# Kernel optimization log

Hardware: AMD Instinct MI355X
Metric: run time of the kernel (lower is better)

## Reference

```python
import math
import jax, jax.numpy as jnp
import numpy as np

H = 8  # num_heads


def setup_inputs() -> dict:
    key = jax.random.key(0)
    ks = jax.random.split(key, 9)
    B, N = 2, 4096
    Cc, C, Cs = 512, 512, 128  # in_channels, hidden_size, in_channels//4
    f = lambda k, shp: jax.random.normal(k, shp, dtype=jnp.float32) * 0.02
    return {
        "s": f(ks[0], (B, N, Cc)),
        "h": f(ks[1], (B, N, Cs)),
        "sh": f(ks[2], (B, N, C)),
        "temperature": jnp.full((H, 1, 1), 0.1, jnp.float32),
        "temperature2": jnp.full((H, 1, 1), 0.1, jnp.float32),
        "Wq_c": f(ks[3], (Cc, Cc)),
        "Wq_s": f(ks[4], (C, C)),
        "Wk_c": f(ks[5], (C, C)),
        "Wv_c": f(ks[6], (C, C)),
        "Wk_s": f(ks[7], (C, C)),
        "Wv_s": f(ks[8], (Cs, Cs)),
    }


def reference(s, h, sh, temperature, temperature2, Wq_c, Wq_s, Wk_c, Wv_c, Wk_s, Wv_s):
    B, N, C = sh.shape
    Cc = s.shape[2]
    Cs = h.shape[2]
    dc, d, ds = Cc // H, C // H, Cs // H

    # torch nn.Linear(bias=False): y = x @ W.T ; reshapes replicate torch's
    # direct reshape(B, H, N, d) layout (no (B,N,H,d)+transpose head split).
    q_c = (s @ Wq_c.T).reshape(B, H, N, dc).swapaxes(-1, -2)  # (B,H,dc,N)
    q_s = (sh @ Wq_s.T).reshape(B, H, N, d)
    k_c = (sh @ Wk_c.T).reshape(B, H, N, d)
    v_c = (sh @ Wv_c.T).reshape(B, H, N, d)
    k_s = (sh @ Wk_s.T).reshape(B, H, N, d)
    v_s = (h @ Wv_s.T).reshape(B, H, N, ds)

    # Channel branch: (B,H,dc,N) @ (B,H,N,d) -> (B,H,dc,d)
    attn_ca = (q_c @ k_c) / math.sqrt(d) * temperature
    attn_ca = jax.nn.softmax(attn_ca, axis=-1)
    x_ca = (attn_ca @ v_c.swapaxes(-2, -1)).reshape(B, N, Cc)  # (B,H,dc,N)->(B,N,Cc)

    # Spatial branch: (B,H,N,d) @ (B,H,d,N) -> (B,H,N,N)
    attn_sa = (q_s @ k_s.swapaxes(-2, -1)) / math.sqrt(d) * temperature2
    attn_sa = jax.nn.softmax(attn_sa, axis=-1)
    x_sa = (attn_sa @ v_s).reshape(B, N, Cs)  # (B,H,N,ds)->(B,N,Cs)

    return jnp.concatenate([x_ca, x_sa], axis=2)  # (B,N,Cc+Cs)
```

## Files before the change

kernel.cpp:

```cpp
#include <hip/hip_runtime.h>


typedef __attribute__((ext_vector_type(8))) __bf16 bf16x8;
typedef __attribute__((ext_vector_type(4))) __bf16 bf16x4;
typedef __attribute__((ext_vector_type(4))) float  f32x4;
typedef __attribute__((ext_vector_type(4))) short  s16x4;

#define LOG2E 1.44269504088896340736f

static __device__ __forceinline__ int is_bf16_io(const unsigned* p)
{
    const unsigned w = p[0];
    return (w >> 16) == (w & 0xffffu);
}

static __device__ __forceinline__ f32x4 mfma16(bf16x4 a, bf16x4 b, f32x4 c)
{
#if __has_builtin(__builtin_amdgcn_mfma_f32_16x16x16bf16_1k)
    union { bf16x4 h; s16x4 s; } ua, ub;
    ua.h = a; ub.h = b;
    return __builtin_amdgcn_mfma_f32_16x16x16bf16_1k(ua.s, ub.s, c, 0, 0, 0);
#elif __has_builtin(__builtin_amdgcn_mfma_f32_16x16x16_bf16)
    return __builtin_amdgcn_mfma_f32_16x16x16_bf16(a, b, c, 0, 0, 0);
#else
    asm("v_mfma_f32_16x16x16_bf16 %0, %1, %2, %0" : "+v"(c) : "v"(a), "v"(b));
    return c;
#endif
}

struct ProjArgs {
    const void* X[6];
    const void* W[6];
    __bf16*     Y[6];
    int         K[6];
    int         yofs[7];
    int         ng;
};

__global__ __launch_bounds__(256) void proj_gemm(ProjArgs args,
                                                 const unsigned* __restrict__ tw)
{
    __shared__ __align__(16) union ShMem {
        struct { __bf16 A[2][128][72]; __bf16 B[2][128][72]; } s;
        __bf16 C[4][64][72];
    } sm;

    const int bf = is_bf16_io(tw);
    const int by = blockIdx.y;
    int g = 0;
    while (by >= args.yofs[g + 1]) ++g;
    const int n0 = (by - args.yofs[g]) * 128;
    const int N  = (args.yofs[g + 1] - args.yofs[g]) * 128;
    const int K  = args.K[g];
    const void* X = args.X[g];
    const void* W = args.W[g];
    __bf16*     Y = args.Y[g];

    const int m0 = blockIdx.x * 128;
    const int t = threadIdx.x;
    const int wave = t >> 6, lane = t & 63;
    const int wr = (wave >> 1) * 64, wc = (wave & 1) * 64;
    const int m16 = lane & 15, quad = lane >> 4;

    f32x4 acc[4][4];
#pragma unroll
    for (int i = 0; i < 4; ++i)
#pragma unroll
        for (int j = 0; j < 4; ++j) acc[i][j] = (f32x4){0.f, 0.f, 0.f, 0.f};

    if (bf) {
        const __bf16* Xb = (const __bf16*)X;
        const __bf16* Wb = (const __bf16*)W;
        bf16x8 pa[4], pb[4];
        auto load = [&](int k0) {
#pragma unroll
            for (int i = 0; i < 4; ++i) {
                const int idx = t + i * 256, row = idx >> 3, off = (idx & 7) * 8;
                pa[i] = *(const bf16x8*)(Xb + (size_t)(m0 + row) * K + k0 + off);
            }
#pragma unroll
            for (int i = 0; i < 4; ++i) {
                const int idx = t + i * 256, row = idx >> 3, off = (idx & 7) * 8;
                pb[i] = *(const bf16x8*)(Wb + (size_t)(n0 + row) * K + k0 + off);
            }
        };
        auto store = [&](int bi) {
#pragma unroll
            for (int i = 0; i < 4; ++i) {
                const int idx = t + i * 256, row = idx >> 3, off = (idx & 7) * 8;
                *(bf16x8*)&sm.s.A[bi][row][off] = pa[i];
            }
#pragma unroll
            for (int i = 0; i < 4; ++i) {
                const int idx = t + i * 256, row = idx >> 3, off = (idx & 7) * 8;
                *(bf16x8*)&sm.s.B[bi][row][off] = pb[i];
            }
        };
        load(0);
        store(0);
        if (64 < K) load(64);
        __syncthreads();
        int step = 0;
        for (int k0 = 0; k0 < K; k0 += 64, ++step) {
            const int cur = step & 1;
            if (k0 + 64 < K)  store(cur ^ 1);
            if (k0 + 128 < K) load(k0 + 128);
#pragma unroll
            for (int kc = 0; kc < 2; ++kc) {
                const int ko = kc * 32 + quad * 8;
                bf16x8 a[4], b[4];
#pragma unroll
                for (int i = 0; i < 4; ++i) a[i] = *(const bf16x8*)&sm.s.A[cur][wr + i * 16 + m16][ko];
#pragma unroll
                for (int j = 0; j < 4; ++j) b[j] = *(const bf16x8*)&sm.s.B[cur][wc + j * 16 + m16][ko];
#pragma unroll
                for (int i = 0; i < 4; ++i)
#pragma unroll
                    for (int j = 0; j < 4; ++j)
                        acc[i][j] = __builtin_amdgcn_mfma_f32_16x16x32_bf16(a[i], b[j], acc[i][j], 0, 0, 0);
            }
            __syncthreads();
        }
    } else {
        const float* Xf = (const float*)X;
        const float* Wf = (const float*)W;
        f32x4 pa[8], pb[8];
        auto load = [&](int k0) {
#pragma unroll
            for (int i = 0; i < 8; ++i) {
                const int idx = t + i * 256, row = idx >> 4, c = (idx & 15) * 4;
                pa[i] = *(const f32x4*)(Xf + (size_t)(m0 + row) * K + k0 + c);
            }
#pragma unroll
            for (int i = 0; i < 8; ++i) {
                const int idx = t + i * 256, row = idx >> 4, c = (idx & 15) * 4;
                pb[i] = *(const f32x4*)(Wf + (size_t)(n0 + row) * K + k0 + c);
            }
        };
        auto store = [&](int bi) {
#pragma unroll
            for (int i = 0; i < 8; ++i) {
                const int idx = t + i * 256, row = idx >> 4, c = (idx & 15) * 4;
                bf16x4 ha;
#pragma unroll
                for (int e = 0; e < 4; ++e) ha[e] = (__bf16)pa[i][e];
                *(bf16x4*)&sm.s.A[bi][row][c] = ha;
            }
#pragma unroll
            for (int i = 0; i < 8; ++i) {
                const int idx = t + i * 256, row = idx >> 4, c = (idx & 15) * 4;
                bf16x4 hb;
#pragma unroll
                for (int e = 0; e < 4; ++e) hb[e] = (__bf16)pb[i][e];
                *(bf16x4*)&sm.s.B[bi][row][c] = hb;
            }
        };
        load(0);
        store(0);
        if (64 < K) load(64);
        __syncthreads();
        int step = 0;
        for (int k0 = 0; k0 < K; k0 += 64, ++step) {
            const int cur = step & 1;
            if (k0 + 64 < K)  store(cur ^ 1);
            if (k0 + 128 < K) load(k0 + 128);
#pragma unroll
            for (int kc = 0; kc < 2; ++kc) {
                const int ko = kc * 32 + quad * 8;
                bf16x8 a[4], b[4];
#pragma unroll
                for (int i = 0; i < 4; ++i) a[i] = *(const bf16x8*)&sm.s.A[cur][wr + i * 16 + m16][ko];
#pragma unroll
                for (int j = 0; j < 4; ++j) b[j] = *(const bf16x8*)&sm.s.B[cur][wc + j * 16 + m16][ko];
#pragma unroll
                for (int i = 0; i < 4; ++i)
#pragma unroll
                    for (int j = 0; j < 4; ++j)
                        acc[i][j] = __builtin_amdgcn_mfma_f32_16x16x32_bf16(a[i], b[j], acc[i][j], 0, 0, 0);
            }
            __syncthreads();
        }
    }

#pragma unroll
    for (int i = 0; i < 4; ++i)
#pragma unroll
        for (int j = 0; j < 4; ++j)
#pragma unroll
            for (int r = 0; r < 4; ++r)
                sm.C[wave][i * 16 + quad * 4 + r][j * 16 + m16] = (__bf16)acc[i][j][r];
#pragma unroll
    for (int p = 0; p < 8; ++p) {
        const int row = p * 8 + (lane >> 3);
        const int c8  = (lane & 7) * 8;
        bf16x8 v = *(const bf16x8*)&sm.C[wave][row][c8];
        *(bf16x8*)&Y[(size_t)(m0 + wr + row) * N + n0 + wc + c8] = v;
    }
}

__global__ __launch_bounds__(256) void zero_f32(float* __restrict__ p, int n)
{
    const int i = blockIdx.x * 256 + threadIdx.x;
    if (i < n) p[i] = 0.f;
}

template <int ATOMIC>
__global__ __launch_bounds__(256) void chan_qk(const __bf16* __restrict__ Qc,
                                               const __bf16* __restrict__ Kc,
                                               float* __restrict__ S)
{
    __shared__ __align__(16) __bf16 Qt[64][136];
    __shared__ __align__(16) __bf16 Kt[64][136];
    const int bx = blockIdx.x;
    const int bh = bx >> 5, split = bx & 31;
    const int b = bh >> 3, hh = bh & 7;
    const int n0 = split * 128;
    const int t = threadIdx.x;
    const size_t base = ((size_t)b * 4096 + (size_t)hh * 512) * 512;

    for (int idx = t; idx < 1024; idx += 256) {
        const int row = idx >> 3, c0 = (idx & 7) * 8;
        bf16x8 q = *(const bf16x8*)(Qc + base + (size_t)(n0 + row) * 64 + c0);
        bf16x8 k = *(const bf16x8*)(Kc + base + (size_t)(n0 + row) * 64 + c0);
#pragma unroll
        for (int e = 0; e < 8; ++e) {
            Qt[c0 + e][row] = q[e];
            Kt[c0 + e][row] = k[e];
        }
    }
    __syncthreads();

    const int wave = t >> 6, lane = t & 63;
    const int m16 = lane & 15, quad = lane >> 4;

    f32x4 acc[4];
#pragma unroll
    for (int tj = 0; tj < 4; ++tj) acc[tj] = (f32x4){0.f, 0.f, 0.f, 0.f};

#pragma unroll
    for (int ks = 0; ks < 4; ++ks) {
        const int ko = ks * 32 + quad * 8;
        bf16x8 af = *(const bf16x8*)&Qt[wave * 16 + m16][ko];
#pragma unroll
        for (int tj = 0; tj < 4; ++tj) {
            bf16x8 bfr = *(const bf16x8*)&Kt[tj * 16 + m16][ko];
            acc[tj] = __builtin_amdgcn_mfma_f32_16x16x32_bf16(af, bfr, acc[tj], 0, 0, 0);
        }
    }

    if (ATOMIC) {
        float* Sb = S + (size_t)bh * 4096;
#pragma unroll
        for (int tj = 0; tj < 4; ++tj)
#pragma unroll
            for (int r = 0; r < 4; ++r)
                atomicAdd(&Sb[(wave * 16 + quad * 4 + r) * 64 + tj * 16 + m16], acc[tj][r]);
    } else {
        float* Sp = S + (size_t)bx * 4096;
#pragma unroll
        for (int tj = 0; tj < 4; ++tj)
#pragma unroll
            for (int r = 0; r < 4; ++r)
                Sp[(wave * 16 + quad * 4 + r) * 64 + tj * 16 + m16] = acc[tj][r];
    }
}

template <int NSPLIT>
__global__ __launch_bounds__(256) void chan_softmax(const float* __restrict__ S,
                                                    const void* __restrict__ temp,
                                                    __bf16* __restrict__ P)
{
    const int bfio = is_bf16_io((const unsigned*)temp);
    const int row = blockIdx.x * 4 + (threadIdx.x >> 6);
    const int bh = row >> 6, i = row & 63;
    const int hh = bh & 7;
    const int j = threadIdx.x & 63;
    const float tv = bfio ? (float)((const __bf16*)temp)[hh] : ((const float*)temp)[hh];
    const float scale = 0.125f * tv;

    float v;
    if (NSPLIT > 1) {
        const float* p = S + ((size_t)bh * NSPLIT) * 4096 + (size_t)i * 64 + j;
        float s = 0.f;
#pragma unroll
        for (int sp = 0; sp < NSPLIT; ++sp) s += p[(size_t)sp * 4096];
        v = s * scale;
    } else {
        v = S[(size_t)bh * 4096 + (size_t)i * 64 + j] * scale;
    }
    float mx = v;
#pragma unroll
    for (int d = 1; d < 64; d <<= 1) mx = fmaxf(mx, __shfl_xor(mx, d, 64));
    const float e = __builtin_amdgcn_exp2f((v - mx) * LOG2E);
    float sum = e;
#pragma unroll
    for (int d = 1; d < 64; d <<= 1) sum += __shfl_xor(sum, d, 64);
    P[(size_t)bh * 4096 + (size_t)i * 64 + j] = (__bf16)(e / sum);
}

__global__ __launch_bounds__(256) void chan_av(const __bf16* __restrict__ P,
                                               const __bf16* __restrict__ Vc,
                                               void* __restrict__ out,
                                               const unsigned* __restrict__ tw)
{
    __shared__ __align__(16) __bf16 Pl[64][72];
    __shared__ __align__(16) __bf16 Vl[64][72];
    const int bf = is_bf16_io(tw);
    const int bx = blockIdx.x;
    const int bh = bx >> 6, ch = bx & 63;
    const int b = bh >> 3, hh = bh & 7;
    const int n0 = ch * 64;
    const int t = threadIdx.x, wave = t >> 6, lane = t & 63;
    const int m16 = lane & 15, quad = lane >> 4;
    const size_t base = ((size_t)b * 4096 + (size_t)hh * 512) * 512;
    const __bf16* Pb = P + (size_t)bh * 4096;

    {
        const int idx0 = t, row0 = idx0 >> 3, off0 = (idx0 & 7) * 8;
        const int idx1 = t + 256, row1 = idx1 >> 3, off1 = (idx1 & 7) * 8;
        *(bf16x8*)&Pl[row0][off0] = *(const bf16x8*)(Pb + (size_t)row0 * 64 + off0);
        *(bf16x8*)&Pl[row1][off1] = *(const bf16x8*)(Pb + (size_t)row1 * 64 + off1);
        *(bf16x8*)&Vl[row0][off0] = *(const bf16x8*)(Vc + base + (size_t)(n0 + row0) * 64 + off0);
        *(bf16x8*)&Vl[row1][off1] = *(const bf16x8*)(Vc + base + (size_t)(n0 + row1) * 64 + off1);
    }
    __syncthreads();

    bf16x8 a[2];
#pragma unroll
    for (int kc = 0; kc < 2; ++kc)
        a[kc] = *(const bf16x8*)&Pl[wave * 16 + m16][kc * 32 + quad * 8];

    f32x4 acc[4];
#pragma unroll
    for (int nt = 0; nt < 4; ++nt) {
        acc[nt] = (f32x4){0.f, 0.f, 0.f, 0.f};
        bf16x8 bv[2];
#pragma unroll
        for (int kc = 0; kc < 2; ++kc)
            bv[kc] = *(const bf16x8*)&Vl[nt * 16 + m16][kc * 32 + quad * 8];
#pragma unroll
        for (int kc = 0; kc < 2; ++kc)
            acc[nt] = __builtin_amdgcn_mfma_f32_16x16x32_bf16(a[kc], bv[kc], acc[nt], 0, 0, 0);
    }

#pragma unroll
    for (int nt = 0; nt < 4; ++nt) {
        const int n = n0 + nt * 16 + m16;
#pragma unroll
        for (int r = 0; r < 4; ++r) {
            const int i = wave * 16 + quad * 4 + r;
            const size_t addr = (size_t)b * 2621440
                              + (size_t)(hh * 512 + i * 8 + (n >> 9)) * 640 + (n & 511);
            if (bf) ((__bf16*)out)[addr] = (__bf16)acc[nt][r];
            else    ((float*)out)[addr]  = acc[nt][r];
        }
    }
}

template <int PATH>
__global__ __launch_bounds__(512) void flash_sa(const __bf16* __restrict__ Qs,
                                                const __bf16* __restrict__ Ks,
                                                const __bf16* __restrict__ Vs,
                                                const void* __restrict__ temp2,
                                                void* __restrict__ out,
                                                float* __restrict__ po,
                                                float* __restrict__ pl)
{
    __shared__ __align__(16) __bf16 Kl[2][64][72];
    __shared__ __align__(16) __bf16 Vt[2][16][72];
    const int bf = is_bf16_io((const unsigned*)temp2);
    const int bid = blockIdx.x;
    const int qt = bid & 15;
    const int bh = bid >> 4;
    const int b = bh >> 3, hh = bh & 7;
    const int nspl = gridDim.y;
    const int spl  = blockIdx.y;
    const int nkt  = 64 / nspl;
    const int kt0  = spl * nkt;
    const int t = threadIdx.x, wave = t >> 6, lane = t & 63;
    const int m16 = lane & 15, quad = lane >> 4;
    const size_t base  = ((size_t)b * 4096 + (size_t)hh * 512) * 512;
    const size_t vbase = ((size_t)b * 4096 + (size_t)hh * 512) * 128;
    const float tv = bf ? (float)((const __bf16*)temp2)[hh] : ((const float*)temp2)[hh];
    const float sl = 0.125f * tv * LOG2E;

    bf16x8 qa[2][2];
#pragma unroll
    for (int g = 0; g < 2; ++g) {
        const int qrow = qt * 256 + g * 128 + wave * 16 + m16;
#pragma unroll
        for (int kc = 0; kc < 2; ++kc) {
            bf16x8 raw = *(const bf16x8*)(Qs + base + (size_t)qrow * 64 + kc * 32 + quad * 8);
#pragma unroll
            for (int e = 0; e < 8; ++e) qa[g][kc][e] = (__bf16)((float)raw[e] * sl);
        }
    }

    bf16x4 ones;
#pragma unroll
    for (int e = 0; e < 4; ++e) ones[e] = (__bf16)1.0f;

    const int krow = t >> 3, koff = (t & 7) * 8;
    const bool vact = t < 256;
    const int vrow = t & 63, vcq = (t >> 6) & 3;
    bf16x8 pk;
    bf16x4 pv;
    auto pref = [&](int kt) {
        pk = *(const bf16x8*)(Ks + base + (size_t)(kt * 64 + krow) * 64 + koff);
        if (vact) pv = *(const bf16x4*)(Vs + vbase + (size_t)(kt * 64 + vrow) * 16 + vcq * 4);
    };
    auto stage = [&](int bi) {
        *(bf16x8*)&Kl[bi][krow][koff] = pk;
        if (vact) {
#pragma unroll
            for (int e = 0; e < 4; ++e) Vt[bi][vcq * 4 + e][vrow] = pv[e];
        }
    };

    pref(kt0);
    stage(0);
    pref(kt0 + 1);
    __syncthreads();

    f32x4 o[2]  = {(f32x4){0.f, 0.f, 0.f, 0.f}, (f32x4){0.f, 0.f, 0.f, 0.f}};
    f32x4 o2[2] = {(f32x4){0.f, 0.f, 0.f, 0.f}, (f32x4){0.f, 0.f, 0.f, 0.f}};

    for (int kk = 0; kk < nkt; ++kk) {
        const int cur = kk & 1;

        bf16x8 kb[4][2];
        bf16x4 vb16[4];
#pragma unroll
        for (int ct = 0; ct < 4; ++ct)
#pragma unroll
            for (int kc = 0; kc < 2; ++kc)
                kb[ct][kc] = *(const bf16x8*)&Kl[cur][ct * 16 + m16][kc * 32 + quad * 8];
#pragma unroll
        for (int ct = 0; ct < 4; ++ct)
            vb16[ct] = *(const bf16x4*)&Vt[cur][m16][ct * 16 + quad * 4];

        if (kk + 1 < nkt) stage(cur ^ 1);
        if (kk + 2 < nkt) pref(kt0 + kk + 2);

#pragma unroll
        for (int g = 0; g < 2; ++g) {
            f32x4 st[4];
#pragma unroll
            for (int ct = 0; ct < 4; ++ct) {
                st[ct] = (f32x4){0.f, 0.f, 0.f, 0.f};
#pragma unroll
                for (int kc = 0; kc < 2; ++kc)
                    st[ct] = __builtin_amdgcn_mfma_f32_16x16x32_bf16(kb[ct][kc], qa[g][kc], st[ct], 0, 0, 0);
            }
#pragma unroll
            for (int ct = 0; ct < 4; ++ct) {
                bf16x4 pe;
#pragma unroll
                for (int r = 0; r < 4; ++r)
                    pe[r] = (__bf16)__builtin_amdgcn_exp2f(st[ct][r]);
                o[g]  = mfma16(pe, vb16[ct], o[g]);
                o2[g] = mfma16(pe, ones,     o2[g]);
            }
        }
        __syncthreads();
    }

    asm volatile("s_nop 7\n\ts_nop 7");

    if (nspl == 1) {
#pragma unroll
        for (int g = 0; g < 2; ++g) {
#pragma unroll
            for (int r = 0; r < 4; ++r) {
                const int n = qt * 256 + g * 128 + wave * 16 + quad * 4 + r;
                const float val = o[g][r] / o2[g][r];
                const size_t addr = (size_t)b * 2621440
                                  + (size_t)(hh * 512 + (n >> 3)) * 640 + 512 + (n & 7) * 16 + m16;
                if (bf) ((__bf16*)out)[addr] = (__bf16)val;
                else    ((float*)out)[addr]  = val;
            }
        }
    } else {
#pragma unroll
        for (int g = 0; g < 2; ++g) {
#pragma unroll
            for (int r = 0; r < 4; ++r) {
                const int n = qt * 256 + g * 128 + wave * 16 + quad * 4 + r;
                const size_t rowi = ((size_t)spl * 16 + bh) * 4096 + n;
                po[rowi * 16 + m16] = o[g][r];
                if (m16 == 0) pl[rowi] = o2[g][r];
            }
        }
    }
}

__global__ __launch_bounds__(256) void flash_combine(const float* __restrict__ po,
                                                     const float* __restrict__ pl,
                                                     void* __restrict__ out,
                                                     const unsigned* __restrict__ tw,
                                                     int nspl)
{
    const int bf = is_bf16_io(tw);
    const int tid = blockIdx.x * 256 + threadIdx.x;
    const int bh = tid >> 12, n = tid & 4095;
    const int b = bh >> 3, hh = bh & 7;

    f32x4 acc[4];
#pragma unroll
    for (int q = 0; q < 4; ++q) acc[q] = (f32x4){0.f, 0.f, 0.f, 0.f};
    float l = 0.f;
    for (int sp = 0; sp < nspl; ++sp) {
        const size_t rowi = ((size_t)sp * 16 + bh) * 4096 + n;
        const f32x4* r = (const f32x4*)(po + rowi * 16);
#pragma unroll
        for (int q = 0; q < 4; ++q) {
            const f32x4 v = r[q];
#pragma unroll
            for (int e = 0; e < 4; ++e) acc[q][e] += v[e];
        }
        l += pl[rowi];
    }
    const float inv = 1.f / l;
    const size_t addr = (size_t)b * 2621440
                      + (size_t)(hh * 512 + (n >> 3)) * 640 + 512 + (n & 7) * 16;
    if (bf) {
#pragma unroll
        for (int q = 0; q < 2; ++q) {
            bf16x8 w;
#pragma unroll
            for (int e = 0; e < 8; ++e) w[e] = (__bf16)(acc[q * 2 + (e >> 2)][e & 3] * inv);
            *(bf16x8*)((__bf16*)out + addr + q * 8) = w;
        }
    } else {
#pragma unroll
        for (int q = 0; q < 4; ++q) {
            f32x4 w;
#pragma unroll
            for (int e = 0; e < 4; ++e) w[e] = acc[q][e] * inv;
            *(f32x4*)((float*)out + addr + q * 4) = w;
        }
    }
}

extern "C" void kernel_launch(void* const* d_in, const int* in_sizes, int n_in,
                              void* d_out, int out_size, void* d_ws, size_t ws_size,
                              hipStream_t stream)
{
    const void* s    = d_in[0];
    const void* h_   = d_in[1];
    const void* sh   = d_in[2];
    const void* t1   = d_in[3];
    const void* t2   = d_in[4];
    const void* Wq_c = d_in[5];
    const void* Wq_s = d_in[6];
    const void* Wk_c = d_in[7];
    const void* Wv_c = d_in[8];
    const void* Wk_s = d_in[9];
    const void* Wv_s = d_in[10];

    const unsigned* t1w = (const unsigned*)t1;
    const dim3 blk(256);
    const size_t PROJ = 4194304;

    const size_t WIDE_BYTES = 5 * PROJ * 2 + 1048576 * 2 + 65536 * 4 + 65536 * 2 + 256;
    const size_t QK_BYTES = 512ull * 4096 * 4;

    if (ws_size >= WIDE_BYTES) {
        __bf16* qc = (__bf16*)d_ws;
        __bf16* kc = qc + PROJ;
        __bf16* vc = kc + PROJ;
        __bf16* qs = vc + PROJ;
        __bf16* ks = qs + PROJ;
        __bf16* vs = ks + PROJ;
        float*  Sb = (float*)(vs + 1048576);
        __bf16* Pb = (__bf16*)(Sb + 65536);

        ProjArgs pa{};
        const void* Xs[6] = {s, sh, sh, sh, sh, h_};
        const void* Ws[6] = {Wq_c, Wk_c, Wv_c, Wq_s, Wk_s, Wv_s};
        __bf16*     Ys[6] = {qc, kc, vc, qs, ks, vs};
        const int   Ks_[6] = {512, 512, 512, 512, 512, 128};
        const int   yt[6] = {4, 4, 4, 4, 4, 1};
        pa.ng = 6;
        int ofs = 0;
        for (int g = 0; g < 6; ++g) {
            pa.X[g] = Xs[g]; pa.W[g] = Ws[g]; pa.Y[g] = Ys[g]; pa.K[g] = Ks_[g];
            pa.yofs[g] = ofs; ofs += yt[g];
        }
        pa.yofs[6] = ofs;

        proj_gemm<<<dim3(64, 21), blk, 0, stream>>>(pa, t1w);

        if (ws_size >= WIDE_BYTES + QK_BYTES) {
            float* qkscr = (float*)((char*)d_ws + WIDE_BYTES);
            chan_qk<0><<<dim3(512), blk, 0, stream>>>(qc, kc, qkscr);
            chan_softmax<32><<<dim3(256), blk, 0, stream>>>(qkscr, t1, Pb);
        } else {
            zero_f32<<<dim3(256), blk, 0, stream>>>(Sb, 65536);
            chan_qk<1><<<dim3(512), blk, 0, stream>>>(qc, kc, Sb);
            chan_softmax<1><<<dim3(256), blk, 0, stream>>>(Sb, t1, Pb);
        }
        chan_av<<<dim3(1024), blk, 0, stream>>>(Pb, vc, d_out, t1w);
        float* po = (float*)qc;
        float* pl = po + 4ull * 1048576;
        flash_sa<0><<<dim3(256, 4), dim3(512), 0, stream>>>(qs, ks, vs, t2, d_out, po, pl);
        flash_combine<<<dim3(256), blk, 0, stream>>>(po, pl, d_out, t1w, 4);
    } else {
        __bf16* A  = (__bf16*)d_ws;
        __bf16* Bf = A + PROJ;
        __bf16* D  = Bf + PROJ;
        float*  Sb = (float*)(D + 1048576);
        __bf16* Pb = (__bf16*)(Sb + 65536);
        int*  flag = (int*)(Pb + 65536);
        (void)flag;

        auto mk2 = [&](const void* X0, const void* W0, __bf16* Y0, int K0, int t0,
                       const void* X1, const void* W1, __bf16* Y1, int K1, int t1_) {
            ProjArgs p{};
            p.ng = 2;
            p.X[0] = X0; p.W[0] = W0; p.Y[0] = Y0; p.K[0] = K0;
            p.X[1] = X1; p.W[1] = W1; p.Y[1] = Y1; p.K[1] = K1;
            p.yofs[0] = 0; p.yofs[1] = t0; p.yofs[2] = t0 + t1_;
            return p;
        };

        const size_t fb_end = (size_t)((char*)(Pb + 65536) + 4 - (char*)d_ws);
        const size_t pofs = (fb_end + 255) & ~(size_t)255;
        const size_t per_split = (1048576 + 65536) * 4;
        int nspl = 1;
        if (ws_size >= pofs + 4 * per_split)      nspl = 4;
        else if (ws_size >= pofs + 2 * per_split) nspl = 2;
        const bool qk_part = (ws_size >= pofs + QK_BYTES);
        float* scratch = (float*)((char*)d_ws + pofs);

        ProjArgs p1 = mk2(s,  Wq_c, A,  512, 4, sh, Wk_c, Bf, 512, 4);
        proj_gemm<<<dim3(64, 8), blk, 0, stream>>>(p1, t1w);
        if (qk_part) {
            chan_qk<0><<<dim3(512), blk, 0, stream>>>(A, Bf, scratch);
            chan_softmax<32><<<dim3(256), blk, 0, stream>>>(scratch, t1, Pb);
        } else {
            zero_f32<<<dim3(256), blk, 0, stream>>>(Sb, 65536);
            chan_qk<1><<<dim3(512), blk, 0, stream>>>(A, Bf, Sb);
            chan_softmax<1><<<dim3(256), blk, 0, stream>>>(Sb, t1, Pb);
        }

        ProjArgs p2 = mk2(sh, Wv_c, A, 512, 4, sh, Wq_s, Bf, 512, 4);
        proj_gemm<<<dim3(64, 8), blk, 0, stream>>>(p2, t1w);
        chan_av<<<dim3(1024), blk, 0, stream>>>(Pb, A, d_out, t1w);

        ProjArgs p3 = mk2(sh, Wk_s, A, 512, 4, h_, Wv_s, D, 128, 1);
        proj_gemm<<<dim3(64, 5), blk, 0, stream>>>(p3, t1w);

        float* po = scratch;
        float* pl = po + (size_t)nspl * 1048576;
        flash_sa<1><<<dim3(256, nspl), dim3(512), 0, stream>>>(Bf, A, D, t2, d_out, po, pl);
        if (nspl > 1)
            flash_combine<<<dim3(256), blk, 0, stream>>>(po, pl, d_out, t1w, nspl);
    }
}
```

Before: 214.7 us.

## Fuse channel AV and spatial flash attention into one launch; swizzle proj blocks

Merges the chan_av and flash_sa kernels into a single av_flash launch. The first 256 x-blocks run flash attention and the remaining blocks each run two chan_av units, one per 256-thread half, sharing a union of shared memory. This removes a launch boundary and lets the small AV work fill CUs alongside flash blocks. It also remaps proj_gemm block indices with an XCD-aware swizzle so that neighbouring tiles land on the same XCD for better L2 reuse. The cost is higher shared-memory and register footprint for the AV blocks, which now run under 512-thread launch bounds.

```diff
diff --git a/kernel.cpp b/kernel.cpp
--- a/kernel.cpp
+++ b/kernel.cpp
@@ -46,7 +46,16 @@
     } sm;
 
     const int bf = is_bf16_io(tw);
-    const int by = blockIdx.y;
+
+    const int nwg = gridDim.x * gridDim.y;
+    int flat = blockIdx.y * gridDim.x + blockIdx.x;
+    if ((nwg & 7) == 0) {
+        const int cpx = nwg >> 3;
+        flat = (flat & 7) * cpx + (flat >> 3);
+    }
+    const int by = flat >> 6;
+    const int bx = flat & 63;
+
     int g = 0;
     while (by >= args.yofs[g + 1]) ++g;
     const int n0 = (by - args.yofs[g]) * 128;
@@ -56,7 +65,7 @@
     const void* W = args.W[g];
     __bf16*     Y = args.Y[g];
 
-    const int m0 = blockIdx.x * 128;
+    const int m0 = bx * 128;
     const int t = threadIdx.x;
     const int wave = t >> 6, lane = t & 63;
     const int wr = (wave >> 1) * 64, wc = (wave & 1) * 64;
@@ -298,37 +307,35 @@
     P[(size_t)bh * 4096 + (size_t)i * 64 + j] = (__bf16)(e / sum);
 }
 
-__global__ __launch_bounds__(256) void chan_av(const __bf16* __restrict__ P,
+struct AvSm { __bf16 Pl[64][72]; __bf16 Vl[64][72]; };
+
+static __device__ __forceinline__ void av_body(AvSm& smav, int unit, int t2,
+                                               const __bf16* __restrict__ P,
                                                const __bf16* __restrict__ Vc,
-                                               void* __restrict__ out,
-                                               const unsigned* __restrict__ tw)
-{
-    __shared__ __align__(16) __bf16 Pl[64][72];
-    __shared__ __align__(16) __bf16 Vl[64][72];
-    const int bf = is_bf16_io(tw);
-    const int bx = blockIdx.x;
-    const int bh = bx >> 6, ch = bx & 63;
+                                               void* __restrict__ out, int bf)
+{
+    const int bh = unit >> 6, ch = unit & 63;
     const int b = bh >> 3, hh = bh & 7;
     const int n0 = ch * 64;
-    const int t = threadIdx.x, wave = t >> 6, lane = t & 63;
+    const int wave = t2 >> 6, lane = t2 & 63;
     const int m16 = lane & 15, quad = lane >> 4;
     const size_t base = ((size_t)b * 4096 + (size_t)hh * 512) * 512;
     const __bf16* Pb = P + (size_t)bh * 4096;
 
     {
-        const int idx0 = t, row0 = idx0 >> 3, off0 = (idx0 & 7) * 8;
-        const int idx1 = t + 256, row1 = idx1 >> 3, off1 = (idx1 & 7) * 8;
-        *(bf16x8*)&Pl[row0][off0] = *(const bf16x8*)(Pb + (size_t)row0 * 64 + off0);
-        *(bf16x8*)&Pl[row1][off1] = *(const bf16x8*)(Pb + (size_t)row1 * 64 + off1);
-        *(bf16x8*)&Vl[row0][off0] = *(const bf16x8*)(Vc + base + (size_t)(n0 + row0) * 64 + off0);
-        *(bf16x8*)&Vl[row1][off1] = *(const bf16x8*)(Vc + base + (size_t)(n0 + row1) * 64 + off1);
+        const int idx0 = t2, row0 = idx0 >> 3, off0 = (idx0 & 7) * 8;
+        const int idx1 = t2 + 256, row1 = idx1 >> 3, off1 = (idx1 & 7) * 8;
+        *(bf16x8*)&smav.Pl[row0][off0] = *(const bf16x8*)(Pb + (size_t)row0 * 64 + off0);
+        *(bf16x8*)&smav.Pl[row1][off1] = *(const bf16x8*)(Pb + (size_t)row1 * 64 + off1);
+        *(bf16x8*)&smav.Vl[row0][off0] = *(const bf16x8*)(Vc + base + (size_t)(n0 + row0) * 64 + off0);
+        *(bf16x8*)&smav.Vl[row1][off1] = *(const bf16x8*)(Vc + base + (size_t)(n0 + row1) * 64 + off1);
     }
     __syncthreads();
 
     bf16x8 a[2];
 #pragma unroll
     for (int kc = 0; kc < 2; ++kc)
-        a[kc] = *(const bf16x8*)&Pl[wave * 16 + m16][kc * 32 + quad * 8];
+        a[kc] = *(const bf16x8*)&smav.Pl[wave * 16 + m16][kc * 32 + quad * 8];
 
     f32x4 acc[4];
 #pragma unroll
@@ -337,7 +344,7 @@
         bf16x8 bv[2];
 #pragma unroll
         for (int kc = 0; kc < 2; ++kc)
-            bv[kc] = *(const bf16x8*)&Vl[nt * 16 + m16][kc * 32 + quad * 8];
+            bv[kc] = *(const bf16x8*)&smav.Vl[nt * 16 + m16][kc * 32 + quad * 8];
 #pragma unroll
         for (int kc = 0; kc < 2; ++kc)
             acc[nt] = __builtin_amdgcn_mfma_f32_16x16x32_bf16(a[kc], bv[kc], acc[nt], 0, 0, 0);
@@ -357,24 +364,29 @@
     }
 }
 
-template <int PATH>
-__global__ __launch_bounds__(512) void flash_sa(const __bf16* __restrict__ Qs,
-                                                const __bf16* __restrict__ Ks,
-                                                const __bf16* __restrict__ Vs,
-                                                const void* __restrict__ temp2,
-                                                void* __restrict__ out,
-                                                float* __restrict__ po,
-                                                float* __restrict__ pl)
-{
-    __shared__ __align__(16) __bf16 Kl[2][64][72];
-    __shared__ __align__(16) __bf16 Vt[2][16][72];
-    const int bf = is_bf16_io((const unsigned*)temp2);
-    const int bid = blockIdx.x;
+__global__ __launch_bounds__(256) void chan_av(const __bf16* __restrict__ P,
+                                               const __bf16* __restrict__ Vc,
+                                               void* __restrict__ out,
+                                               const unsigned* __restrict__ tw)
+{
+    __shared__ __align__(16) AvSm smav;
+    av_body(smav, blockIdx.x, threadIdx.x, P, Vc, out, is_bf16_io(tw));
+}
+
+struct FlashSm { __bf16 Kl[2][64][72]; __bf16 Vt[2][16][72]; };
+
+static __device__ __forceinline__ void flash_body(FlashSm& smf, int bid, int spl, int nspl,
+                                                  const __bf16* __restrict__ Qs,
+                                                  const __bf16* __restrict__ Ks,
+                                                  const __bf16* __restrict__ Vs,
+                                                  const void* __restrict__ temp2,
+                                                  void* __restrict__ out,
+                                                  float* __restrict__ po,
+                                                  float* __restrict__ pl, int bf)
+{
     const int qt = bid & 15;
     const int bh = bid >> 4;
     const int b = bh >> 3, hh = bh & 7;
-    const int nspl = gridDim.y;
-    const int spl  = blockIdx.y;
     const int nkt  = 64 / nspl;
     const int kt0  = spl * nkt;
     const int t = threadIdx.x, wave = t >> 6, lane = t & 63;
@@ -410,10 +422,10 @@
         if (vact) pv = *(const bf16x4*)(Vs + vbase + (size_t)(kt * 64 + vrow) * 16 + vcq * 4);
     };
     auto stage = [&](int bi) {
-        *(bf16x8*)&Kl[bi][krow][koff] = pk;
+        *(bf16x8*)&smf.Kl[bi][krow][koff] = pk;
         if (vact) {
 #pragma unroll
-            for (int e = 0; e < 4; ++e) Vt[bi][vcq * 4 + e][vrow] = pv[e];
+            for (int e = 0; e < 4; ++e) smf.Vt[bi][vcq * 4 + e][vrow] = pv[e];
         }
     };
 
@@ -434,10 +446,10 @@
         for (int ct = 0; ct < 4; ++ct)
 #pragma unroll
             for (int kc = 0; kc < 2; ++kc)
-                kb[ct][kc] = *(const bf16x8*)&Kl[cur][ct * 16 + m16][kc * 32 + quad * 8];
+                kb[ct][kc] = *(const bf16x8*)&smf.Kl[cur][ct * 16 + m16][kc * 32 + quad * 8];
 #pragma unroll
         for (int ct = 0; ct < 4; ++ct)
-            vb16[ct] = *(const bf16x4*)&Vt[cur][m16][ct * 16 + quad * 4];
+            vb16[ct] = *(const bf16x4*)&smf.Vt[cur][m16][ct * 16 + quad * 4];
 
         if (kk + 1 < nkt) stage(cur ^ 1);
         if (kk + 2 < nkt) pref(kt0 + kk + 2);
@@ -491,6 +503,42 @@
                 if (m16 == 0) pl[rowi] = o2[g][r];
             }
         }
+    }
+}
+
+__global__ __launch_bounds__(512) void flash_sa(const __bf16* __restrict__ Qs,
+                                                const __bf16* __restrict__ Ks,
+                                                const __bf16* __restrict__ Vs,
+                                                const void* __restrict__ temp2,
+                                                void* __restrict__ out,
+                                                float* __restrict__ po,
+                                                float* __restrict__ pl)
+{
+    __shared__ __align__(16) FlashSm smf;
+    flash_body(smf, blockIdx.x, blockIdx.y, gridDim.y, Qs, Ks, Vs, temp2, out,
+               po, pl, is_bf16_io((const unsigned*)temp2));
+}
+
+__global__ __launch_bounds__(512) void av_flash(const __bf16* __restrict__ P,
+                                                const __bf16* __restrict__ Vc,
+                                                const __bf16* __restrict__ Qs,
+                                                const __bf16* __restrict__ Ks,
+                                                const __bf16* __restrict__ Vs,
+                                                const void* __restrict__ temp2,
+                                                void* __restrict__ out,
+                                                float* __restrict__ po,
+                                                float* __restrict__ pl,
+                                                const unsigned* __restrict__ tw)
+{
+    __shared__ __align__(16) union { FlashSm f; AvSm a[2]; } sm;
+    const int bf = is_bf16_io(tw);
+    if (blockIdx.x < 256) {
+        flash_body(sm.f, blockIdx.x, blockIdx.y, 4, Qs, Ks, Vs, temp2, out, po, pl, bf);
+    } else {
+        const int half = threadIdx.x >> 8;
+        const int t2 = threadIdx.x & 255;
+        const int unit = ((blockIdx.x - 256) * 4 + blockIdx.y) * 2 + half;
+        av_body(sm.a[half], unit, t2, P, Vc, out, bf);
     }
 }
 
@@ -591,28 +639,32 @@
 
         proj_gemm<<<dim3(64, 21), blk, 0, stream>>>(pa, t1w);
 
-        if (ws_size >= WIDE_BYTES + QK_BYTES) {
+        const bool extra = (ws_size >= WIDE_BYTES + QK_BYTES);
+        if (extra) {
             float* qkscr = (float*)((char*)d_ws + WIDE_BYTES);
             chan_qk<0><<<dim3(512), blk, 0, stream>>>(qc, kc, qkscr);
             chan_softmax<32><<<dim3(256), blk, 0, stream>>>(qkscr, t1, Pb);
+            float* po = (float*)qc;
+            float* pl = qkscr;
+            av_flash<<<dim3(384, 4), dim3(512), 0, stream>>>(
+                Pb, vc, qs, ks, vs, t2, d_out, po, pl, t1w);
+            flash_combine<<<dim3(256), blk, 0, stream>>>(po, pl, d_out, t1w, 4);
         } else {
             zero_f32<<<dim3(256), blk, 0, stream>>>(Sb, 65536);
             chan_qk<1><<<dim3(512), blk, 0, stream>>>(qc, kc, Sb);
             chan_softmax<1><<<dim3(256), blk, 0, stream>>>(Sb, t1, Pb);
-        }
-        chan_av<<<dim3(1024), blk, 0, stream>>>(Pb, vc, d_out, t1w);
-        float* po = (float*)qc;
-        float* pl = po + 4ull * 1048576;
-        flash_sa<0><<<dim3(256, 4), dim3(512), 0, stream>>>(qs, ks, vs, t2, d_out, po, pl);
-        flash_combine<<<dim3(256), blk, 0, stream>>>(po, pl, d_out, t1w, 4);
+            chan_av<<<dim3(1024), blk, 0, stream>>>(Pb, vc, d_out, t1w);
+            float* po = (float*)qc;
+            float* pl = po + 4ull * 1048576;
+            flash_sa<<<dim3(256, 4), dim3(512), 0, stream>>>(qs, ks, vs, t2, d_out, po, pl);
+            flash_combine<<<dim3(256), blk, 0, stream>>>(po, pl, d_out, t1w, 4);
+        }
     } else {
         __bf16* A  = (__bf16*)d_ws;
         __bf16* Bf = A + PROJ;
         __bf16* D  = Bf + PROJ;
         float*  Sb = (float*)(D + 1048576);
         __bf16* Pb = (__bf16*)(Sb + 65536);
-        int*  flag = (int*)(Pb + 65536);
-        (void)flag;
 
         auto mk2 = [&](const void* X0, const void* W0, __bf16* Y0, int K0, int t0,
                        const void* X1, const void* W1, __bf16* Y1, int K1, int t1_) {
@@ -653,7 +705,7 @@
 
         float* po = scratch;
         float* pl = po + (size_t)nspl * 1048576;
-        flash_sa<1><<<dim3(256, nspl), dim3(512), 0, stream>>>(Bf, A, D, t2, d_out, po, pl);
+        flash_sa<<<dim3(256, nspl), dim3(512), 0, stream>>>(Bf, A, D, t2, d_out, po, pl);
         if (nspl > 1)
             flash_combine<<<dim3(256), blk, 0, stream>>>(po, pl, d_out, t1w, nspl);
     }
```

Measured after the change: 227.5 us. 5.9% more time.
